# Performance work log

Measured on AMD Instinct MI355X. Metric: run time of the kernel, lower is better.

Reference implementation:

```python
import jax, jax.numpy as jnp
import numpy as np

N = 500_000
D = 128
NUM_SEGMENTS = 4096


def setup_inputs() -> dict:
    key = jax.random.key(0)
    k1, k2, k3 = jax.random.split(key, 3)
    feat = jax.random.normal(k1, (N, D), dtype=jnp.float32)
    # xavier_uniform for Linear(D -> 1): bound = sqrt(6 / (D + 1))
    bound = float(np.sqrt(6.0 / (D + 1)))
    gate_w = jax.random.uniform(k2, (D, 1), dtype=jnp.float32, minval=-bound, maxval=bound)
    gate_b = jnp.zeros((1,), dtype=jnp.float32)
    segment_ids = jnp.sort(jax.random.randint(k3, (N,), 0, NUM_SEGMENTS, dtype=jnp.int64))
    return {
        "feat": feat,
        "gate_w": gate_w,
        "gate_b": gate_b,
        "segment_ids": segment_ids,
        "num_segments": NUM_SEGMENTS,
    }


def reference(feat, gate_w, gate_b, segment_ids, num_segments):
    # gate_nn: Linear(D -> 1), gate shape [N, 1] -> squeeze to [N]
    gate = (feat @ gate_w + gate_b)[:, 0]                      # [N]
    # segment softmax over nodes of each graph (stable)
    seg_max = jax.ops.segment_max(gate, segment_ids, num_segments=num_segments)  # [G]
    e = jnp.exp(gate - seg_max[segment_ids])                   # [N]
    denom = jax.ops.segment_sum(e, segment_ids, num_segments=num_segments)       # [G]
    alpha = e / denom[segment_ids]                             # [N]
    # weighted segment sum readout: [G, D]
    readout = jax.ops.segment_sum(feat * alpha[:, None], segment_ids,
                                  num_segments=num_segments)
    return readout
```

## Files before the change

kernel.cpp:

```cpp
#include <hip/hip_runtime.h>
#include <math.h>

#define NSEG 4096
#define DD   128

__global__ void bounds_kernel(const int* __restrict__ seg,
                              int* __restrict__ seg_start, int N) {
    int i = blockIdx.x * blockDim.x + threadIdx.x;
    int stride = gridDim.x * blockDim.x;
    for (int n = i; n < N; n += stride) {
        int cur  = seg[n];
        int prev = (n == 0) ? -1 : seg[n - 1];
        for (int g = prev + 1; g <= cur; ++g) seg_start[g] = n;
        if (n == N - 1) {
            for (int g = cur + 1; g <= NSEG; ++g) seg_start[g] = N;
        }
    }
}

__global__ __launch_bounds__(256) void fused_kernel(
        const float* __restrict__ feat,
        const float* __restrict__ gw,
        const float* __restrict__ gb,
        const int*  __restrict__ seg_start,
        float* __restrict__ out) {
    __shared__ float  gs[2][16];
    __shared__ float4 red[8][32];

    int g   = blockIdx.x;
    int s   = seg_start[g];
    int e   = seg_start[g + 1];
    int len = e - s;

    int tid = threadIdx.x;
    int rg  = tid >> 5;
    int c   = tid & 31;

    const float4* f4 = (const float4*)feat;
    float4 w4 = ((const float4*)gw)[c];
    float  b0 = gb[0];

    float  m   = -INFINITY;
    float  l   = 0.0f;
    float4 acc = {0.f, 0.f, 0.f, 0.f};

    int nt = (len + 15) >> 4;

    float4 va = {0.f,0.f,0.f,0.f}, vb = {0.f,0.f,0.f,0.f};
    {
        int n1 = s + rg, n2 = n1 + 8;
        if (n1 < e) va = f4[n1 * 32 + c];
        if (n2 < e) vb = f4[n2 * 32 + c];
    }

    for (int t = 0; t < nt; ++t) {
        int base = s + t * 16;
        int n1 = base + rg, n2 = n1 + 8;
        float4 ca = va, cb = vb;

        int p1 = n1 + 16, p2 = n2 + 16;
        va = make_float4(0.f,0.f,0.f,0.f);
        vb = make_float4(0.f,0.f,0.f,0.f);
        if (p1 < e) va = f4[p1 * 32 + c];
        if (p2 < e) vb = f4[p2 * 32 + c];

        float d1 = ca.x*w4.x + ca.y*w4.y + ca.z*w4.z + ca.w*w4.w;
        float d2 = cb.x*w4.x + cb.y*w4.y + cb.z*w4.z + cb.w*w4.w;
        #pragma unroll
        for (int off = 16; off; off >>= 1) {
            d1 += __shfl_xor(d1, off);
            d2 += __shfl_xor(d2, off);
        }
        if (c == 0) {
            gs[t & 1][rg]     = (n1 < e) ? d1 + b0 : -INFINITY;
            gs[t & 1][rg + 8] = (n2 < e) ? d2 + b0 : -INFINITY;
        }
        __syncthreads();

        float gj = gs[t & 1][tid & 15];
        float tmax = gj;
        #pragma unroll
        for (int off = 8; off; off >>= 1) tmax = fmaxf(tmax, __shfl_xor(tmax, off));
        float m_new = fmaxf(m, tmax);
        float scale = __expf(m - m_new);
        float pj = __expf(gj - m_new);
        float psum = pj;
        #pragma unroll
        for (int off = 8; off; off >>= 1) psum += __shfl_xor(psum, off);
        l = l * scale + psum;

        float pa = __expf(gs[t & 1][rg]     - m_new);
        float pb = __expf(gs[t & 1][rg + 8] - m_new);
        acc.x = acc.x * scale + pa * ca.x + pb * cb.x;
        acc.y = acc.y * scale + pa * ca.y + pb * cb.y;
        acc.z = acc.z * scale + pa * ca.z + pb * cb.z;
        acc.w = acc.w * scale + pa * ca.w + pb * cb.w;
        m = m_new;
    }

    red[rg][c] = acc;
    __syncthreads();
    if (rg == 0) {
        float4 r = red[0][c];
        #pragma unroll
        for (int k = 1; k < 8; ++k) {
            float4 v = red[k][c];
            r.x += v.x; r.y += v.y; r.z += v.z; r.w += v.w;
        }
        float invl = (len > 0) ? 1.0f / l : 0.0f;
        r.x *= invl; r.y *= invl; r.z *= invl; r.w *= invl;
        ((float4*)out)[g * 32 + c] = r;
    }
}

extern "C" void kernel_launch(void* const* d_in, const int* in_sizes, int n_in,
                              void* d_out, int out_size, void* d_ws, size_t ws_size,
                              hipStream_t stream) {
    const float* feat = (const float*)d_in[0];
    const float* gw   = (const float*)d_in[1];
    const float* gb   = (const float*)d_in[2];
    const int*   seg  = (const int*)d_in[3];
    int N = in_sizes[0] / DD;

    int* seg_start = (int*)d_ws;

    bounds_kernel<<<1024, 256, 0, stream>>>(seg, seg_start, N);
    fused_kernel<<<NSEG, 256, 0, stream>>>(feat, gw, gb, seg_start, (float*)d_out);
}
```

Measured before the change: 53.24 us.

## Fuse segment bounds via binary search and deepen per-tile prefetch

Removes the separate bounds kernel and has each block binary-search the sorted segment ids for its own start and end, which drops one kernel launch and a global round trip. The tile grows from 16 to 32 rows, so each warp keeps four rows in flight, the number of per-tile barriers halves, and more loads overlap. Feature loads become nontemporal to avoid polluting the cache with streamed data. In exchange, every block performs two serial binary searches of about 19 dependent loads each, and register pressure rises.

```diff
diff --git a/kernel.cpp b/kernel.cpp
--- a/kernel.cpp
+++ b/kernel.cpp
@@ -4,112 +4,115 @@
 #define NSEG 4096
 #define DD   128
 
-__global__ void bounds_kernel(const int* __restrict__ seg,
-                              int* __restrict__ seg_start, int N) {
-    int i = blockIdx.x * blockDim.x + threadIdx.x;
-    int stride = gridDim.x * blockDim.x;
-    for (int n = i; n < N; n += stride) {
-        int cur  = seg[n];
-        int prev = (n == 0) ? -1 : seg[n - 1];
-        for (int g = prev + 1; g <= cur; ++g) seg_start[g] = n;
-        if (n == N - 1) {
-            for (int g = cur + 1; g <= NSEG; ++g) seg_start[g] = N;
-        }
+typedef float f4 __attribute__((ext_vector_type(4)));
+
+__device__ __forceinline__ int lower_bound(const int* __restrict__ seg, int N, int g) {
+    int lo = 0, hi = N;
+    while (lo < hi) {
+        int mid = (lo + hi) >> 1;
+        if (seg[mid] < g) lo = mid + 1; else hi = mid;
     }
+    return lo;
 }
 
 __global__ __launch_bounds__(256) void fused_kernel(
         const float* __restrict__ feat,
         const float* __restrict__ gw,
         const float* __restrict__ gb,
-        const int*  __restrict__ seg_start,
+        const int*  __restrict__ seg,
+        int N,
         float* __restrict__ out) {
-    __shared__ float  gs[2][16];
-    __shared__ float4 red[8][32];
+    __shared__ float gs[2][32];
+    __shared__ f4    red[8][32];
 
-    int g   = blockIdx.x;
-    int s   = seg_start[g];
-    int e   = seg_start[g + 1];
+    int g = blockIdx.x;
+    int s = lower_bound(seg, N, g);
+    int e = lower_bound(seg, N, g + 1);
     int len = e - s;
 
     int tid = threadIdx.x;
     int rg  = tid >> 5;
     int c   = tid & 31;
 
-    const float4* f4 = (const float4*)feat;
-    float4 w4 = ((const float4*)gw)[c];
-    float  b0 = gb[0];
+    const f4* fp = (const f4*)feat;
+    f4    w4 = ((const f4*)gw)[c];
+    float b0 = gb[0];
 
-    float  m   = -INFINITY;
-    float  l   = 0.0f;
-    float4 acc = {0.f, 0.f, 0.f, 0.f};
+    float m = -INFINITY, l = 0.0f;
+    f4 acc = {0.f, 0.f, 0.f, 0.f};
 
-    int nt = (len + 15) >> 4;
+    int ntiles = (len + 31) >> 5;
 
-    float4 va = {0.f,0.f,0.f,0.f}, vb = {0.f,0.f,0.f,0.f};
+    f4 va = {0,0,0,0}, vb = {0,0,0,0}, vc = {0,0,0,0}, vd = {0,0,0,0};
     {
-        int n1 = s + rg, n2 = n1 + 8;
-        if (n1 < e) va = f4[n1 * 32 + c];
-        if (n2 < e) vb = f4[n2 * 32 + c];
+        int n1 = s + rg;
+        if (n1      < e) va = __builtin_nontemporal_load(&fp[(n1     ) * 32 + c]);
+        if (n1 + 8  < e) vb = __builtin_nontemporal_load(&fp[(n1 + 8 ) * 32 + c]);
+        if (n1 + 16 < e) vc = __builtin_nontemporal_load(&fp[(n1 + 16) * 32 + c]);
+        if (n1 + 24 < e) vd = __builtin_nontemporal_load(&fp[(n1 + 24) * 32 + c]);
     }
 
-    for (int t = 0; t < nt; ++t) {
-        int base = s + t * 16;
-        int n1 = base + rg, n2 = n1 + 8;
-        float4 ca = va, cb = vb;
+    for (int t = 0; t < ntiles; ++t) {
+        int base = s + t * 32;
+        int n1 = base + rg;
+        f4 ca = va, cb = vb, cc = vc, cd = vd;
 
-        int p1 = n1 + 16, p2 = n2 + 16;
-        va = make_float4(0.f,0.f,0.f,0.f);
-        vb = make_float4(0.f,0.f,0.f,0.f);
-        if (p1 < e) va = f4[p1 * 32 + c];
-        if (p2 < e) vb = f4[p2 * 32 + c];
+        int p1 = n1 + 32;
+        va = (f4){0,0,0,0}; vb = (f4){0,0,0,0}; vc = (f4){0,0,0,0}; vd = (f4){0,0,0,0};
+        if (p1      < e) va = __builtin_nontemporal_load(&fp[(p1     ) * 32 + c]);
+        if (p1 + 8  < e) vb = __builtin_nontemporal_load(&fp[(p1 + 8 ) * 32 + c]);
+        if (p1 + 16 < e) vc = __builtin_nontemporal_load(&fp[(p1 + 16) * 32 + c]);
+        if (p1 + 24 < e) vd = __builtin_nontemporal_load(&fp[(p1 + 24) * 32 + c]);
 
         float d1 = ca.x*w4.x + ca.y*w4.y + ca.z*w4.z + ca.w*w4.w;
         float d2 = cb.x*w4.x + cb.y*w4.y + cb.z*w4.z + cb.w*w4.w;
+        float d3 = cc.x*w4.x + cc.y*w4.y + cc.z*w4.z + cc.w*w4.w;
+        float d4 = cd.x*w4.x + cd.y*w4.y + cd.z*w4.z + cd.w*w4.w;
         #pragma unroll
         for (int off = 16; off; off >>= 1) {
             d1 += __shfl_xor(d1, off);
             d2 += __shfl_xor(d2, off);
+            d3 += __shfl_xor(d3, off);
+            d4 += __shfl_xor(d4, off);
         }
+        int buf = t & 1;
         if (c == 0) {
-            gs[t & 1][rg]     = (n1 < e) ? d1 + b0 : -INFINITY;
-            gs[t & 1][rg + 8] = (n2 < e) ? d2 + b0 : -INFINITY;
+            gs[buf][rg]      = (n1      < e) ? d1 + b0 : -INFINITY;
+            gs[buf][rg + 8]  = (n1 + 8  < e) ? d2 + b0 : -INFINITY;
+            gs[buf][rg + 16] = (n1 + 16 < e) ? d3 + b0 : -INFINITY;
+            gs[buf][rg + 24] = (n1 + 24 < e) ? d4 + b0 : -INFINITY;
         }
         __syncthreads();
 
-        float gj = gs[t & 1][tid & 15];
+        float gj = gs[buf][tid & 31];
         float tmax = gj;
         #pragma unroll
-        for (int off = 8; off; off >>= 1) tmax = fmaxf(tmax, __shfl_xor(tmax, off));
+        for (int off = 16; off; off >>= 1) tmax = fmaxf(tmax, __shfl_xor(tmax, off));
         float m_new = fmaxf(m, tmax);
         float scale = __expf(m - m_new);
         float pj = __expf(gj - m_new);
         float psum = pj;
         #pragma unroll
-        for (int off = 8; off; off >>= 1) psum += __shfl_xor(psum, off);
+        for (int off = 16; off; off >>= 1) psum += __shfl_xor(psum, off);
         l = l * scale + psum;
 
-        float pa = __expf(gs[t & 1][rg]     - m_new);
-        float pb = __expf(gs[t & 1][rg + 8] - m_new);
-        acc.x = acc.x * scale + pa * ca.x + pb * cb.x;
-        acc.y = acc.y * scale + pa * ca.y + pb * cb.y;
-        acc.z = acc.z * scale + pa * ca.z + pb * cb.z;
-        acc.w = acc.w * scale + pa * ca.w + pb * cb.w;
+        float pa = __expf(gs[buf][rg]      - m_new);
+        float pb = __expf(gs[buf][rg + 8]  - m_new);
+        float pc = __expf(gs[buf][rg + 16] - m_new);
+        float pd = __expf(gs[buf][rg + 24] - m_new);
+        acc = acc * scale + pa * ca + pb * cb + pc * cc + pd * cd;
         m = m_new;
     }
 
     red[rg][c] = acc;
     __syncthreads();
     if (rg == 0) {
-        float4 r = red[0][c];
+        f4 r = red[0][c];
         #pragma unroll
-        for (int k = 1; k < 8; ++k) {
-            float4 v = red[k][c];
-            r.x += v.x; r.y += v.y; r.z += v.z; r.w += v.w;
-        }
+        for (int k = 1; k < 8; ++k) r += red[k][c];
         float invl = (len > 0) ? 1.0f / l : 0.0f;
-        r.x *= invl; r.y *= invl; r.z *= invl; r.w *= invl;
-        ((float4*)out)[g * 32 + c] = r;
+        r *= invl;
+        ((f4*)out)[g * 32 + c] = r;
     }
 }
 
@@ -122,8 +125,5 @@
     const int*   seg  = (const int*)d_in[3];
     int N = in_sizes[0] / DD;
 
-    int* seg_start = (int*)d_ws;
-
-    bounds_kernel<<<1024, 256, 0, stream>>>(seg, seg_start, N);
-    fused_kernel<<<NSEG, 256, 0, stream>>>(feat, gw, gb, seg_start, (float*)d_out);
+    fused_kernel<<<NSEG, 256, 0, stream>>>(feat, gw, gb, seg, N, (float*)d_out);
 }
```

Measured after the change: 50.69 us. 1.05x faster.
